# Optimization experiments

Hardware: AMD Instinct MI355X
Metric: run time of the kernel (lower is better)

## Reference

```python
import jax, jax.numpy as jnp
import numpy as np

B, S, D = 2, 1024, 4096
N_HEADS, KV_HEADS, HEAD_DIM = 32, 8, 128
EPS = 1e-6
ROPE_THETA = 1e6


def setup_inputs() -> dict:
    key = jax.random.key(0)
    ks = jax.random.split(key, 7)
    scale = 0.02
    x = jax.random.normal(ks[0], (B, S, D), dtype=jnp.float32)
    positions = jnp.broadcast_to(jnp.arange(S, dtype=jnp.int32)[None, :], (B, S))
    wq = jax.random.normal(ks[1], (D, N_HEADS, HEAD_DIM), dtype=jnp.float32) * scale
    wk = jax.random.normal(ks[2], (D, KV_HEADS, HEAD_DIM), dtype=jnp.float32) * scale
    wv = jax.random.normal(ks[3], (D, KV_HEADS, HEAD_DIM), dtype=jnp.float32) * scale
    wo = jax.random.normal(ks[4], (N_HEADS, HEAD_DIM, D), dtype=jnp.float32) * scale
    q_norm_w = 1.0 + jax.random.normal(ks[5], (HEAD_DIM,), dtype=jnp.float32) * 0.01
    k_norm_w = 1.0 + jax.random.normal(ks[6], (HEAD_DIM,), dtype=jnp.float32) * 0.01
    return {"x": x, "positions": positions, "wq": wq, "wk": wk, "wv": wv,
            "wo": wo, "q_norm_w": q_norm_w, "k_norm_w": k_norm_w}


def _rms_norm(t, w):
    # per-head RMSNorm over last (head_dim) axis
    var = jnp.mean(jnp.square(t), axis=-1, keepdims=True)
    return (t * jax.lax.rsqrt(var + EPS)) * w


def _rope(t, positions):
    # neox-style rotary embedding; t: [B, S, n, H], positions: [B, S]
    half = t.shape[-1] // 2
    inv_freq = 1.0 / (ROPE_THETA ** (jnp.arange(0, half, dtype=jnp.float32) / half))
    ang = positions.astype(jnp.float32)[..., None] * inv_freq  # [B, S, half]
    cos = jnp.cos(ang)[:, :, None, :]  # [B, S, 1, half]
    sin = jnp.sin(ang)[:, :, None, :]
    t1, t2 = t[..., :half], t[..., half:]
    return jnp.concatenate([t1 * cos - t2 * sin, t2 * cos + t1 * sin], axis=-1)


def reference(x, positions, wq, wk, wv, wo, q_norm_w, k_norm_w):
    # QKV projections (einsum layers: 'bsd,dnh->bsnh')
    q = jnp.einsum('bsd,dnh->bsnh', x, wq)  # [B, S, N, H]
    k = jnp.einsum('bsd,dkh->bskh', x, wk)  # [B, S, K, H]
    v = jnp.einsum('bsd,dkh->bskh', x, wv)
    # per-head QK RMSNorm, then RoPE
    q = _rope(_rms_norm(q, q_norm_w), positions)
    k = _rope(_rms_norm(k, k_norm_w), positions)
    # GQA: expand KV heads to query heads
    groups = N_HEADS // KV_HEADS
    k = jnp.repeat(k, groups, axis=2)  # [B, S, N, H]
    v = jnp.repeat(v, groups, axis=2)
    sm_scale = HEAD_DIM ** -0.5
    scores = jnp.einsum('bqnh,btnh->bnqt', q, k) * sm_scale  # [B, N, S, S]
    causal = jnp.tril(jnp.ones((S, S), dtype=bool))
    scores = jnp.where(causal[None, None], scores, jnp.finfo(scores.dtype).min)
    probs = jax.nn.softmax(scores, axis=-1)
    attn = jnp.einsum('bnqt,btnh->bqnh', probs, v)  # [B, S, N, H]
    out = jnp.einsum('bqnh,nhd->bqd', attn, wo)  # output projection
    return out
```

## Files before the change

kernel.cpp:

```cpp
#include <hip/hip_runtime.h>
#include <stdint.h>

#define S_LEN   1024
#define D_MODEL 4096
#define NHQ     32
#define NKV     8
#define HD      128
#define NTOK    2048
#define NQKV    6144
#define SM_SCALE 0.08838834764831843f

typedef __attribute__((ext_vector_type(8))) __bf16 bf16x8;
typedef __attribute__((ext_vector_type(4))) float f32x4;

__device__ __forceinline__ unsigned short f2bf(float f) {
  union { float f; unsigned u; } x; x.f = f;
  unsigned r = x.u + 0x7fffu + ((x.u >> 16) & 1u);
  return (unsigned short)(r >> 16);
}
__device__ __forceinline__ float bf2f(unsigned short u) {
  union { unsigned u; float f; } x; x.u = (unsigned)u << 16; return x.f;
}

__device__ __forceinline__ void gload_lds16(const void* g, void* l) {
  __builtin_amdgcn_global_load_lds((__attribute__((address_space(1))) void*)g,
                                   (__attribute__((address_space(3))) void*)l,
                                   16, 0, 0);
}

__global__ void k_f32_to_bf16(const float* __restrict__ in,
                              unsigned short* __restrict__ out, int n8) {
  int i = blockIdx.x * blockDim.x + threadIdx.x;
  if (i >= n8) return;
  const float4* p = (const float4*)(in + (size_t)i * 8);
  float4 v0 = p[0], v1 = p[1];
  uint4 o;
  o.x = f2bf(v0.x) | ((unsigned)f2bf(v0.y) << 16);
  o.y = f2bf(v0.z) | ((unsigned)f2bf(v0.w) << 16);
  o.z = f2bf(v1.x) | ((unsigned)f2bf(v1.y) << 16);
  o.w = f2bf(v1.z) | ((unsigned)f2bf(v1.w) << 16);
  *(uint4*)(out + (size_t)i * 8) = o;
}

__global__ void k_transpose(const float* __restrict__ in,
                            unsigned short* __restrict__ out, int R, int C) {
  __shared__ float t[32][33];
  int c = threadIdx.x & 31, r0 = threadIdx.x >> 5;
  int cb = blockIdx.x * 32, rb = blockIdx.y * 32;
#pragma unroll
  for (int i = 0; i < 4; ++i) {
    int r = r0 + i * 8;
    t[r][c] = in[(size_t)(rb + r) * C + cb + c];
  }
  __syncthreads();
#pragma unroll
  for (int i = 0; i < 4; ++i) {
    int r = r0 + i * 8;
    out[(size_t)(cb + r) * R + rb + c] = f2bf(t[c][r]);
  }
}


#define LGKM0 { asm volatile("s_waitcnt lgkmcnt(0)" ::: "memory"); \
                __builtin_amdgcn_sched_barrier(0); }
#define SCHED __builtin_amdgcn_sched_barrier(0);
#define BAR   __builtin_amdgcn_s_barrier();
#define GATE  { if constexpr (NF == 4)                                          \
                  asm volatile("s_waitcnt vmcnt(4)" ::: "memory");              \
                else                                                            \
                  asm volatile("s_waitcnt vmcnt(3)" ::: "memory"); }

#define STGA(h, bufb, kOff)                                                     \
  _Pragma("unroll")                                                             \
  for (int i_ = 0; i_ < 2; ++i_)                                                \
    gload_lds16(gA[i_] + (kOff) + (h) * 64,                                     \
                smem + (bufb) + (h) * 16384 + dA[i_]);

#define STGB(h, bufb, kOff)                                                     \
  _Pragma("unroll")                                                             \
  for (int i_ = 0; i_ < NF / 2; ++i_)                                           \
    gload_lds16(gB[i_] + (kOff) + (h) * 64,                                     \
                smem + (bufb) + 32768 + (h) * (NF * 4096) + dB[i_]);

#define RD_A(dst, mh, kh, bufb)                                                 \
  _Pragma("unroll")                                                             \
  for (int mf = 0; mf < 4; ++mf) {                                              \
    int row = wr * 128 + (mh) * 64 + mf * 16 + lr;                              \
    dst[mf] = *(const bf16x8*)(smem + (bufb) + (kh) * 16384 + row * 64          \
                               + ((lg * 16) ^ (((row >> 1) & 3) << 4)));        \
  }

#define RD_B(dst, kh, bufb)                                                     \
  _Pragma("unroll")                                                             \
  for (int nf = 0; nf < NF; ++nf) {                                             \
    int row = wc * (NF * 16) + nf * 16 + lr;                                    \
    dst[nf] = *(const bf16x8*)(smem + (bufb) + 32768 + (kh) * (NF * 4096)       \
                               + row * 64 + ((lg * 16) ^ (((row >> 1) & 3) << 4))); \
  }

#define MFMA16(mh, AF, BF)                                                      \
  __builtin_amdgcn_s_setprio(1);                                                \
  _Pragma("unroll")                                                             \
  for (int mf = 0; mf < 4; ++mf)                                                \
    _Pragma("unroll")                                                           \
    for (int nf = 0; nf < NF; ++nf)                                             \
      acc[(mh) * 4 + mf][nf] = __builtin_amdgcn_mfma_f32_16x16x32_bf16(         \
          AF[mf], BF[nf], acc[(mh) * 4 + mf][nf], 0, 0, 0);                     \
  __builtin_amdgcn_s_setprio(0);

template <int NF, typename OutT>
__global__ __launch_bounds__(512, 1) void k_gemm256(
    const unsigned short* __restrict__ Aptr,
    const unsigned short* __restrict__ Bptr,
    OutT* __restrict__ C,
    int Kstride, int ldc, int NT, int SGN, int nxn) {
  extern __shared__ __align__(16) char smem[];
  constexpr int BUFST = 32768 + NF * 8192;
  int tid = threadIdx.x;
  int l = tid & 63;
  int w = tid >> 6;
  int lr = l & 15, lg = l >> 4;
  int wr = w >> 2, wc = w & 3;
  int per_xcd = gridDim.x >> 3;
  int x8 = blockIdx.x & 7, i = blockIdx.x >> 3;
  int SGM = per_xcd / SGN;
  int xr = x8 / nxn, xc = x8 - xr * nxn;
  int iy = i / SGN;
  int by = xr * SGM + iy, bx = xc * SGN + (i - iy * SGN);
  int bm = by * 256, bn = bx * (NF * 64);

  const char* gA[2]; int dA[2];
#pragma unroll
  for (int i_ = 0; i_ < 2; ++i_) {
    int lin = i_ * 512 + tid;
    int r_ = lin >> 2, slot = lin & 3, sw = slot ^ ((r_ >> 1) & 3);
    gA[i_] = (const char*)(Aptr + (size_t)(bm + r_) * Kstride) + sw * 16;
    dA[i_] = lin * 16;
  }
  const char* gB[NF / 2]; int dB[NF / 2];
#pragma unroll
  for (int i_ = 0; i_ < NF / 2; ++i_) {
    int lin = i_ * 512 + tid;
    int r_ = lin >> 2, slot = lin & 3, sw = slot ^ ((r_ >> 1) & 3);
    gB[i_] = (const char*)(Bptr + (size_t)(bn + r_) * Kstride) + sw * 16;
    dB[i_] = lin * 16;
  }

  f32x4 acc[8][NF] = {};
  bf16x8 afA[4], afB[4], bfA[NF], bfB[NF];

  STGA(0, 0, 0) STGB(0, 0, 0)
  STGA(1, 0, 0) STGB(1, 0, 0)
  GATE
  BAR
  RD_A(afA, 0, 0, 0) RD_B(bfA, 0, 0)

  for (int kt = 0; kt < NT; ++kt) {
    int curb = (kt & 1) * BUFST;
    int nxtb = BUFST - curb;
    int kOff = (kt + 1) * 128;
    STGA(0, nxtb, kOff)
    BAR LGKM0
    RD_A(afB, 1, 0, curb) SCHED
    MFMA16(0, afA, bfA)
    BAR
    STGB(0, nxtb, kOff)
    GATE BAR LGKM0
    RD_A(afA, 0, 1, curb) RD_B(bfB, 1, curb) SCHED
    MFMA16(1, afB, bfA)
    BAR
    STGA(1, nxtb, kOff)
    BAR LGKM0
    RD_A(afB, 1, 1, curb) SCHED
    MFMA16(0, afA, bfB)
    BAR
    STGB(1, nxtb, kOff)
    GATE BAR LGKM0
    RD_A(afA, 0, 0, nxtb) RD_B(bfA, 0, nxtb) SCHED
    MFMA16(1, afB, bfB)
    BAR
  }

#pragma unroll
  for (int mh = 0; mh < 2; ++mh)
#pragma unroll
    for (int mf = 0; mf < 4; ++mf)
#pragma unroll
      for (int nf = 0; nf < NF; ++nf)
#pragma unroll
        for (int j = 0; j < 4; ++j) {
          size_t idx = (size_t)(bm + wr * 128 + mh * 64 + mf * 16 + lg * 4 + j) * ldc +
                       bn + wc * (NF * 16) + nf * 16 + lr;
          float v = acc[mh * 4 + mf][nf][j];
          if constexpr (sizeof(OutT) == 2) C[idx] = f2bf(v);
          else C[idx] = v;
        }
}

__global__ void k_norm_rope(const unsigned short* __restrict__ qkv,
                            const float* __restrict__ w,
                            const int* __restrict__ positions,
                            unsigned short* __restrict__ out, int nheads, int colbase,
                            float oscale) {
  int wid = blockIdx.x * 4 + (threadIdx.x >> 6);
  int lane = threadIdx.x & 63;
  int token = wid / nheads, head = wid - token * nheads;
  const unsigned short* src = qkv + (size_t)token * NQKV + colbase + head * HD;
  float e0 = bf2f(src[lane]), e1 = bf2f(src[lane + 64]);
  float ss = e0 * e0 + e1 * e1;
#pragma unroll
  for (int m = 1; m < 64; m <<= 1) ss += __shfl_xor(ss, m, 64);
  float rs = rsqrtf(ss * (1.0f / 128.0f) + 1e-6f);
  float n0 = e0 * rs * w[lane], n1 = e1 * rs * w[lane + 64];
  int pos = positions[token];
  float invf = exp2f((float)lane * (-19.931568569324174f / 64.0f));
  float ang = (float)pos * invf;
  float sv, cv;
  sincosf(ang, &sv, &cv);
  float o0 = (n0 * cv - n1 * sv) * oscale;
  float o1 = (n1 * cv + n0 * sv) * oscale;
  int b = token >> 10, s = token & 1023;
  size_t ob = ((size_t)(b * nheads + head) * S_LEN + s) * HD;
  out[ob + lane] = f2bf(o0);
  out[ob + 64 + lane] = f2bf(o1);
}

__global__ void k_v_transpose(const unsigned short* __restrict__ qkv,
                              unsigned short* __restrict__ vt) {
  __shared__ unsigned short t[32][33];
  int slice = blockIdx.z;
  int b = slice >> 3, kh = slice & 7;
  const unsigned short* in = qkv + (size_t)(b * S_LEN) * NQKV + 5120 + kh * HD;
  unsigned short* out = vt + (size_t)slice * HD * S_LEN;
  int c = threadIdx.x & 31, r0 = threadIdx.x >> 5;
  int s0 = blockIdx.y * 32, d0 = blockIdx.x * 32;
#pragma unroll
  for (int i = 0; i < 4; ++i) {
    int r = r0 + i * 8;
    t[r][c] = in[(size_t)(s0 + r) * NQKV + d0 + c];
  }
  __syncthreads();
#pragma unroll
  for (int i = 0; i < 4; ++i) {
    int r = r0 + i * 8;
    out[(size_t)(d0 + r) * S_LEN + s0 + c] = t[c][r];
  }
}

__global__ __launch_bounds__(256) void k_attn(const unsigned short* __restrict__ qh,
                                              const unsigned short* __restrict__ kbuf,
                                              const unsigned short* __restrict__ vtbuf,
                                              unsigned short* __restrict__ attn_out) {
  __shared__ __align__(16) unsigned short k_lds[64 * 128];
  __shared__ __align__(16) unsigned short v_lds[128 * 64];
  __shared__ __align__(16) unsigned short p_lds[4][16 * 64];
  int b = blockIdx.z, h = blockIdx.y, bx = blockIdx.x;
  int khd = h >> 2;
  int tid = threadIdx.x, w = tid >> 6, l = tid & 63;
  int lr = l & 15, lg = l >> 4;
  const unsigned short* K = kbuf + (size_t)(b * NKV + khd) * S_LEN * HD;
  const unsigned short* VT = vtbuf + (size_t)(b * NKV + khd) * HD * S_LEN;
  char* klp = (char*)k_lds;
  char* vlp = (char*)v_lds;
  char* plp = (char*)p_lds[w];
  int swz = (lr & 7) << 4;

  for (int strip = 0; strip < 2; ++strip) {
    int qs = strip ? (15 - bx) : bx;
    int q0 = qs * 64;
    const unsigned short* Q = qh + ((size_t)(b * NHQ + h) * S_LEN + q0 + w * 16) * HD;
    bf16x8 qf[4];
#pragma unroll
    for (int kk = 0; kk < 4; ++kk)
      qf[kk] = *(const bf16x8*)&Q[(size_t)lr * HD + kk * 32 + lg * 8];

    f32x4 o[8] = {};
    float m_[4], l_[4];
#pragma unroll
    for (int j = 0; j < 4; ++j) { m_[j] = -1e30f; l_[j] = 0.0f; }

    int nt = qs + 1;
    for (int t = 0; t < nt; ++t) {
      int t0 = t * 64;
      __syncthreads();
#pragma unroll
      for (int it = 0; it < 4; ++it) {
        int db = (tid + it * 256) * 16;
        int kr = db >> 8, kc = db & 255;
        gload_lds16(K + (size_t)(t0 + kr) * HD + ((kc ^ ((kr & 7) << 4)) >> 1), klp + db);
        int vr = db >> 7, vc = db & 127;
        gload_lds16(VT + (size_t)vr * S_LEN + t0 + ((vc ^ ((vr & 7) << 4)) >> 1), vlp + db);
      }
      __syncthreads();

      f32x4 sc[4];
      __builtin_amdgcn_s_setprio(1);
#pragma unroll
      for (int ct = 0; ct < 4; ++ct) {
        f32x4 s = {};
        int row = ct * 16 + lr;
#pragma unroll
        for (int kk = 0; kk < 4; ++kk) {
          bf16x8 kf = *(const bf16x8*)(klp + row * 256 + ((kk * 64 + lg * 16) ^ swz));
          s = __builtin_amdgcn_mfma_f32_16x16x32_bf16(qf[kk], kf, s, 0, 0, 0);
        }
        sc[ct] = s;
      }
      __builtin_amdgcn_s_setprio(0);

      bool full = (t < qs);
      float alpha[4];
#pragma unroll
      for (int j = 0; j < 4; ++j) {
        if (!full) {
          int rg = q0 + w * 16 + lg * 4 + j;
#pragma unroll
          for (int ct = 0; ct < 4; ++ct)
            sc[ct][j] = (t0 + ct * 16 + lr <= rg) ? sc[ct][j] : -1e30f;
        }
        float mx = fmaxf(fmaxf(sc[0][j], sc[1][j]), fmaxf(sc[2][j], sc[3][j]));
#pragma unroll
        for (int msk = 1; msk < 16; msk <<= 1) mx = fmaxf(mx, __shfl_xor(mx, msk, 64));
        float mn = fmaxf(m_[j], mx);
        alpha[j] = __expf(m_[j] - mn);
        int q = lg * 4 + j;
        int psw = (q & 7) << 4;
        float ps = 0.0f;
#pragma unroll
        for (int ct = 0; ct < 4; ++ct) {
          float p = __expf(sc[ct][j] - mn);
          ps += p;
          *(unsigned short*)(plp + q * 128 + (((ct * 16 + lr) * 2) ^ psw)) = f2bf(p);
        }
#pragma unroll
        for (int msk = 1; msk < 16; msk <<= 1) ps += __shfl_xor(ps, msk, 64);
        l_[j] = l_[j] * alpha[j] + ps;
        m_[j] = mn;
      }
#pragma unroll
      for (int dc = 0; dc < 8; ++dc) {
        o[dc][0] *= alpha[0]; o[dc][1] *= alpha[1];
        o[dc][2] *= alpha[2]; o[dc][3] *= alpha[3];
      }
      asm volatile("s_waitcnt lgkmcnt(0)" ::: "memory");
      __builtin_amdgcn_s_setprio(1);
#pragma unroll
      for (int kt = 0; kt < 2; ++kt) {
        bf16x8 pa = *(const bf16x8*)(plp + lr * 128 + ((kt * 64 + lg * 16) ^ swz));
#pragma unroll
        for (int dc = 0; dc < 8; ++dc) {
          int vrow = dc * 16 + lr;
          bf16x8 vf = *(const bf16x8*)(vlp + vrow * 128 + ((kt * 64 + lg * 16) ^ swz));
          o[dc] = __builtin_amdgcn_mfma_f32_16x16x32_bf16(pa, vf, o[dc], 0, 0, 0);
        }
      }
      __builtin_amdgcn_s_setprio(0);
    }

#pragma unroll
    for (int j = 0; j < 4; ++j) {
      int rg = q0 + w * 16 + lg * 4 + j;
      size_t row = (size_t)(b * S_LEN + rg) * D_MODEL + h * HD;
      float inv = 1.0f / l_[j];
#pragma unroll
      for (int dc = 0; dc < 8; ++dc)
        attn_out[row + dc * 16 + lr] = f2bf(o[dc][j] * inv);
    }
  }
}

extern "C" void kernel_launch(void* const* d_in, const int* in_sizes, int n_in,
                              void* d_out, int out_size, void* d_ws, size_t ws_size,
                              hipStream_t stream) {
  const float* x        = (const float*)d_in[0];
  const int* positions  = (const int*)d_in[1];
  const float* wq       = (const float*)d_in[2];
  const float* wk       = (const float*)d_in[3];
  const float* wv       = (const float*)d_in[4];
  const float* wo       = (const float*)d_in[5];
  const float* qnw      = (const float*)d_in[6];
  const float* knw      = (const float*)d_in[7];
  float* out            = (float*)d_out;

  char* ws = (char*)d_ws;
  unsigned short* xb   = (unsigned short*)(ws);
  unsigned short* wB   = (unsigned short*)(ws + 16777216);
  unsigned short* woT  = (unsigned short*)(ws + 67108864);
  unsigned short* qkvb = (unsigned short*)(ws + 100663296);
  unsigned short* qh   = wB;
  unsigned short* khb  = (unsigned short*)(ws + 33554432);
  unsigned short* vtb  = (unsigned short*)(ws + 37748736);
  unsigned short* attn = xb;

  dim3 tb(256);
  k_f32_to_bf16<<<4096, tb, 0, stream>>>(x, xb, 1048576);
  k_transpose<<<dim3(128, 128), tb, 0, stream>>>(wq, wB, 4096, 4096);
  k_transpose<<<dim3(32, 128), tb, 0, stream>>>(wk, wB + (size_t)4096 * 4096, 4096, 1024);
  k_transpose<<<dim3(32, 128), tb, 0, stream>>>(wv, wB + (size_t)5120 * 4096, 4096, 1024);
  k_transpose<<<dim3(128, 128), tb, 0, stream>>>(wo, woT, 4096, 4096);

  k_gemm256<4, unsigned short><<<dim3(192), dim3(512), 131072, stream>>>(
      xb, wB, qkvb, 4096, 6144, 64, 6, 4);

  k_norm_rope<<<16384, tb, 0, stream>>>(qkvb, qnw, positions, qh, 32, 0, SM_SCALE);
  k_norm_rope<<<4096, tb, 0, stream>>>(qkvb, knw, positions, khb, 8, 4096, 1.0f);
  k_v_transpose<<<dim3(4, 32, 16), tb, 0, stream>>>(qkvb, vtb);

  k_attn<<<dim3(8, 32, 2), tb, 0, stream>>>(qh, khb, vtb, attn);

  k_gemm256<2, float><<<dim3(256), dim3(512), 98304, stream>>>(
      attn, woT, out, 4096, 4096, 64, 8, 4);
}
```

Baseline: 325.5 us.

## Restructure GEMM main loop into two phases with full-height MFMA blocks

The GEMM k-loop goes from four quarter phases (A and B half-tile loads staged separately, 4x NF MFMAs per phase) to two half phases. Each phase stages both A and B for one k-half, reads all 8 A fragments, and issues 8xNF MFMAs. This halves the barriers and waitcnt gates per k-tile and gives longer MFMA runs. In exchange it doubles the A-fragment registers, adding VGPR pressure, and coarsens the overlap between loads and compute.

```diff
diff --git a/kernel.cpp b/kernel.cpp
--- a/kernel.cpp
+++ b/kernel.cpp
@@ -70,24 +70,22 @@
                 else                                                            \
                   asm volatile("s_waitcnt vmcnt(3)" ::: "memory"); }
 
-#define STGA(h, bufb, kOff)                                                     \
+#define STGH(h, bufb, kOff)                                                     \
+  { _Pragma("unroll")                                                           \
+    for (int i_ = 0; i_ < 2; ++i_)                                              \
+      gload_lds16(gA[i_] + (kOff) + (h) * 64,                                   \
+                  smem + (bufb) + (h) * 16384 + dA[i_]);                        \
+    _Pragma("unroll")                                                           \
+    for (int i_ = 0; i_ < NF / 2; ++i_)                                         \
+      gload_lds16(gB[i_] + (kOff) + (h) * 64,                                   \
+                  smem + (bufb) + 32768 + (h) * (NF * 4096) + dB[i_]); }
+
+#define RD_A8(dst, kh, bufb)                                                    \
   _Pragma("unroll")                                                             \
-  for (int i_ = 0; i_ < 2; ++i_)                                                \
-    gload_lds16(gA[i_] + (kOff) + (h) * 64,                                     \
-                smem + (bufb) + (h) * 16384 + dA[i_]);
-
-#define STGB(h, bufb, kOff)                                                     \
-  _Pragma("unroll")                                                             \
-  for (int i_ = 0; i_ < NF / 2; ++i_)                                           \
-    gload_lds16(gB[i_] + (kOff) + (h) * 64,                                     \
-                smem + (bufb) + 32768 + (h) * (NF * 4096) + dB[i_]);
-
-#define RD_A(dst, mh, kh, bufb)                                                 \
-  _Pragma("unroll")                                                             \
-  for (int mf = 0; mf < 4; ++mf) {                                              \
-    int row = wr * 128 + (mh) * 64 + mf * 16 + lr;                              \
-    dst[mf] = *(const bf16x8*)(smem + (bufb) + (kh) * 16384 + row * 64          \
-                               + ((lg * 16) ^ (((row >> 1) & 3) << 4)));        \
+  for (int f = 0; f < 8; ++f) {                                                 \
+    int row = wr * 128 + f * 16 + lr;                                           \
+    dst[f] = *(const bf16x8*)(smem + (bufb) + (kh) * 16384 + row * 64           \
+                              + ((lg * 16) ^ (((row >> 1) & 3) << 4)));         \
   }
 
 #define RD_B(dst, kh, bufb)                                                     \
@@ -98,18 +96,18 @@
                                + row * 64 + ((lg * 16) ^ (((row >> 1) & 3) << 4))); \
   }
 
-#define MFMA16(mh, AF, BF)                                                      \
+#define MFMA32(AF, BF)                                                          \
   __builtin_amdgcn_s_setprio(1);                                                \
   _Pragma("unroll")                                                             \
-  for (int mf = 0; mf < 4; ++mf)                                                \
+  for (int f = 0; f < 8; ++f)                                                   \
     _Pragma("unroll")                                                           \
     for (int nf = 0; nf < NF; ++nf)                                             \
-      acc[(mh) * 4 + mf][nf] = __builtin_amdgcn_mfma_f32_16x16x32_bf16(         \
-          AF[mf], BF[nf], acc[(mh) * 4 + mf][nf], 0, 0, 0);                     \
+      acc[f][nf] = __builtin_amdgcn_mfma_f32_16x16x32_bf16(                     \
+          AF[f], BF[nf], acc[f][nf], 0, 0, 0);                                  \
   __builtin_amdgcn_s_setprio(0);
 
 template <int NF, typename OutT>
-__global__ __launch_bounds__(512, 1) void k_gemm256(
+__global__ __launch_bounds__(512, 1) void k_gemm2ph(
     const unsigned short* __restrict__ Aptr,
     const unsigned short* __restrict__ Bptr,
     OutT* __restrict__ C,
@@ -147,54 +145,42 @@
   }
 
   f32x4 acc[8][NF] = {};
-  bf16x8 afA[4], afB[4], bfA[NF], bfB[NF];
-
-  STGA(0, 0, 0) STGB(0, 0, 0)
-  STGA(1, 0, 0) STGB(1, 0, 0)
+  bf16x8 afA[8], afB[8], bfA[NF], bfB[NF];
+
+  STGH(0, 0, 0)
+  STGH(1, 0, 0)
   GATE
   BAR
-  RD_A(afA, 0, 0, 0) RD_B(bfA, 0, 0)
+  RD_A8(afA, 0, 0) RD_B(bfA, 0, 0)
 
   for (int kt = 0; kt < NT; ++kt) {
     int curb = (kt & 1) * BUFST;
     int nxtb = BUFST - curb;
     int kOff = (kt + 1) * 128;
-    STGA(0, nxtb, kOff)
-    BAR LGKM0
-    RD_A(afB, 1, 0, curb) SCHED
-    MFMA16(0, afA, bfA)
+    STGH(0, nxtb, kOff)
+    GATE BAR LGKM0
+    RD_A8(afB, 1, curb) RD_B(bfB, 1, curb) SCHED
+    MFMA32(afA, bfA)
     BAR
-    STGB(0, nxtb, kOff)
+    STGH(1, nxtb, kOff)
     GATE BAR LGKM0
-    RD_A(afA, 0, 1, curb) RD_B(bfB, 1, curb) SCHED
-    MFMA16(1, afB, bfA)
+    RD_A8(afA, 0, nxtb) RD_B(bfA, 0, nxtb) SCHED
+    MFMA32(afB, bfB)
     BAR
-    STGA(1, nxtb, kOff)
-    BAR LGKM0
-    RD_A(afB, 1, 1, curb) SCHED
-    MFMA16(0, afA, bfB)
-    BAR
-    STGB(1, nxtb, kOff)
-    GATE BAR LGKM0
-    RD_A(afA, 0, 0, nxtb) RD_B(bfA, 0, nxtb) SCHED
-    MFMA16(1, afB, bfB)
-    BAR
-  }
-
-#pragma unroll
-  for (int mh = 0; mh < 2; ++mh)
-#pragma unroll
-    for (int mf = 0; mf < 4; ++mf)
-#pragma unroll
-      for (int nf = 0; nf < NF; ++nf)
-#pragma unroll
-        for (int j = 0; j < 4; ++j) {
-          size_t idx = (size_t)(bm + wr * 128 + mh * 64 + mf * 16 + lg * 4 + j) * ldc +
-                       bn + wc * (NF * 16) + nf * 16 + lr;
-          float v = acc[mh * 4 + mf][nf][j];
-          if constexpr (sizeof(OutT) == 2) C[idx] = f2bf(v);
-          else C[idx] = v;
-        }
+  }
+
+#pragma unroll
+  for (int f = 0; f < 8; ++f)
+#pragma unroll
+    for (int nf = 0; nf < NF; ++nf)
+#pragma unroll
+      for (int j = 0; j < 4; ++j) {
+        size_t idx = (size_t)(bm + wr * 128 + f * 16 + lg * 4 + j) * ldc +
+                     bn + wc * (NF * 16) + nf * 16 + lr;
+        float v = acc[f][nf][j];
+        if constexpr (sizeof(OutT) == 2) C[idx] = f2bf(v);
+        else C[idx] = v;
+      }
 }
 
 __global__ void k_norm_rope(const unsigned short* __restrict__ qkv,
@@ -399,7 +385,7 @@
   k_transpose<<<dim3(32, 128), tb, 0, stream>>>(wv, wB + (size_t)5120 * 4096, 4096, 1024);
   k_transpose<<<dim3(128, 128), tb, 0, stream>>>(wo, woT, 4096, 4096);
 
-  k_gemm256<4, unsigned short><<<dim3(192), dim3(512), 131072, stream>>>(
+  k_gemm2ph<4, unsigned short><<<dim3(192), dim3(512), 131072, stream>>>(
       xb, wB, qkvb, 4096, 6144, 64, 6, 4);
 
   k_norm_rope<<<16384, tb, 0, stream>>>(qkvb, qnw, positions, qh, 32, 0, SM_SCALE);
@@ -408,6 +394,6 @@
 
   k_attn<<<dim3(8, 32, 2), tb, 0, stream>>>(qh, khb, vtb, attn);
 
-  k_gemm256<2, float><<<dim3(256), dim3(512), 98304, stream>>>(
+  k_gemm2ph<2, float><<<dim3(256), dim3(512), 98304, stream>>>(
       attn, woT, out, 4096, 4096, 64, 8, 4);
 }
```

New measurement: 331.5 us. Within noise of the previous version (+1.8%).
